# Performance work log

Measured on AMD Instinct MI355X. Metric: run time of the kernel, lower is better.

The kernel has to match this reference:

```python
import jax, jax.numpy as jnp
import numpy as np

B, N, D, H = 2, 2048, 1024, 16
HD = D // H

def rotate_half(x):
    # pairs (x1,x2) -> (-x2,x1), interleaved along last dim
    x1 = x[..., 0::2]
    x2 = x[..., 1::2]
    return jnp.stack((-x2, x1), axis=-1).reshape(x.shape)

def rope(freqs, t):
    return t * freqs[0] + rotate_half(t) * freqs[1]

def attn(q, k, v):
    scale = q.shape[-1] ** -0.5
    s = jnp.einsum('bhqd,bhkd->bhqk', q, k) * scale
    return jnp.einsum('bhqk,bhkd->bhqd', jax.nn.softmax(s, axis=-1), v)

def layernorm(x, g, b, eps=1e-5):
    m = x.mean(-1, keepdims=True)
    v = x.var(-1, keepdims=True)
    return (x - m) * jax.lax.rsqrt(v + eps) * g + b

def ffn(x, w1, b1, lg, lb, w2, b2):
    h = layernorm(x @ w1 + b1, lg, lb)
    return jax.nn.gelu(h, approximate=False) @ w2 + b2

def self_block(x, enc, wqkv_w, wqkv_b, out_w, out_b, f1w, f1b, lg, lb, f2w, f2b):
    b, n, d = x.shape
    hd = enc.shape[-1]; h = d // hd
    qkv = (x @ wqkv_w + wqkv_b).reshape(b, n, h, hd, 3).transpose(0, 2, 1, 3, 4)  # [b,h,n,hd,3]
    q, k, v = qkv[..., 0], qkv[..., 1], qkv[..., 2]
    q = rope(enc, q)
    k = rope(enc, k)
    ctx = attn(q, k, v).transpose(0, 2, 1, 3).reshape(b, n, d)
    msg = ctx @ out_w + out_b
    return x + ffn(jnp.concatenate([x, msg], -1), f1w, f1b, lg, lb, f2w, f2b)

def cross_block(x0, x1, h, qkw, qkb, vw, vb, ow, ob, f1w, f1b, lg, lb, f2w, f2b):
    b, n, d = x0.shape
    hd = d // h
    def heads(t):
        return t.reshape(b, -1, h, hd).transpose(0, 2, 1, 3)
    qk0 = heads(x0 @ qkw + qkb)
    qk1 = heads(x1 @ qkw + qkb)
    v0 = heads(x0 @ vw + vb)
    v1 = heads(x1 @ vw + vb)
    m0 = attn(qk0, qk1, v1).transpose(0, 2, 1, 3).reshape(b, n, d) @ ow + ob
    m1 = attn(qk1, qk0, v0).transpose(0, 2, 1, 3).reshape(b, n, d) @ ow + ob
    y0 = x0 + ffn(jnp.concatenate([x0, m0], -1), f1w, f1b, lg, lb, f2w, f2b)
    y1 = x1 + ffn(jnp.concatenate([x1, m1], -1), f1w, f1b, lg, lb, f2w, f2b)
    return y0, y1

def setup_inputs() -> dict:
    key = jax.random.key(0)
    ks = iter(jax.random.split(key, 40))
    def w(shape, scale=0.02):
        return (jax.random.normal(next(ks), shape, dtype=jnp.float32) * scale)
    inp = {
        'desc0': jax.random.normal(next(ks), (B, N, D), dtype=jnp.float32),
        'desc1': jax.random.normal(next(ks), (B, N, D), dtype=jnp.float32),
        'encoding0': jax.random.normal(next(ks), (2, B, 1, N, HD), dtype=jnp.float32),
        'encoding1': jax.random.normal(next(ks), (2, B, 1, N, HD), dtype=jnp.float32),
        # self-attention block params
        'wqkv_w': w((D, 3 * D)), 'wqkv_b': w((3 * D,)),
        'sout_w': w((D, D)), 'sout_b': w((D,)),
        'sf1_w': w((2 * D, 2 * D)), 'sf1_b': w((2 * D,)),
        'sln_g': jnp.ones((2 * D,), jnp.float32), 'sln_b': jnp.zeros((2 * D,), jnp.float32),
        'sf2_w': w((2 * D, D)), 'sf2_b': w((D,)),
        # cross-attention block params
        'qk_w': w((D, D)), 'qk_b': w((D,)),
        'v_w': w((D, D)), 'v_b': w((D,)),
        'cout_w': w((D, D)), 'cout_b': w((D,)),
        'cf1_w': w((2 * D, 2 * D)), 'cf1_b': w((2 * D,)),
        'cln_g': jnp.ones((2 * D,), jnp.float32), 'cln_b': jnp.zeros((2 * D,), jnp.float32),
        'cf2_w': w((2 * D, D)), 'cf2_b': w((D,)),
    }
    return inp

def reference(desc0, desc1, encoding0, encoding1,
              wqkv_w, wqkv_b, sout_w, sout_b, sf1_w, sf1_b, sln_g, sln_b, sf2_w, sf2_b,
              qk_w, qk_b, v_w, v_b, cout_w, cout_b, cf1_w, cf1_b, cln_g, cln_b, cf2_w, cf2_b):
    d0 = self_block(desc0, encoding0, wqkv_w, wqkv_b, sout_w, sout_b, sf1_w, sf1_b, sln_g, sln_b, sf2_w, sf2_b)
    d1 = self_block(desc1, encoding1, wqkv_w, wqkv_b, sout_w, sout_b, sf1_w, sf1_b, sln_g, sln_b, sf2_w, sf2_b)
    return cross_block(d0, d1, H, qk_w, qk_b, v_w, v_b, cout_w, cout_b, cf1_w, cf1_b, cln_g, cln_b, cf2_w, cf2_b)
```

## Files before the change

### kernel.cpp

```cpp
#include <hip/hip_runtime.h>


typedef unsigned short u16;
typedef unsigned int u32;
typedef float f32x4 __attribute__((ext_vector_type(4)));
typedef float f32x16 __attribute__((ext_vector_type(16)));
typedef __bf16 bf16x8 __attribute__((ext_vector_type(8)));
typedef u16 u16x2 __attribute__((ext_vector_type(2)));
typedef u16 u16x4 __attribute__((ext_vector_type(4)));
typedef u16 u16x8 __attribute__((ext_vector_type(8)));
typedef u32 u32x4 __attribute__((ext_vector_type(4)));

__device__ __forceinline__ u16 f2b(float f) {
  union { float f; unsigned u; } v; v.f = f;
  unsigned r = v.u + 0x7FFFu + ((v.u >> 16) & 1u);
  return (u16)(r >> 16);
}
__device__ __forceinline__ float b2f(u16 s) {
  union { unsigned u; float f; } v; v.u = ((unsigned)s) << 16;
  return v.f;
}
__device__ __forceinline__ void gload16(const void* g, void* l) {
  __builtin_amdgcn_global_load_lds((const __attribute__((address_space(1))) void*)g,
                                   (__attribute__((address_space(3))) void*)l, 16, 0, 0);
}
__device__ __forceinline__ u32 cvtpk(float lo, float hi) {
  u32 r;
  asm("v_cvt_pk_bf16_f32 %0, %1, %2" : "=v"(r) : "v"(lo), "v"(hi));
  return r;
}
#define MFMA16(a, b, c) __builtin_amdgcn_mfma_f32_16x16x32_bf16(a, b, c, 0, 0, 0)
#define MFMA32(a, b, c) __builtin_amdgcn_mfma_f32_32x32x16_bf16(a, b, c, 0, 0, 0)

__global__ __launch_bounds__(256) void wtrans(const float* __restrict__ src,
                                              u16* __restrict__ dst, int K, int N) {
  __shared__ __align__(16) u16 tile[64][72];
  const int k0 = blockIdx.y * 64, n0 = blockIdx.x * 64;
  const int t = threadIdx.x;
  {
    const int kl = t >> 2, nc = (t & 3) * 16;
    const float* sp = src + (size_t)(k0 + kl) * N + n0 + nc;
#pragma unroll
    for (int j = 0; j < 4; ++j) {
      float4 f = *(const float4*)(sp + j * 4);
      tile[kl][nc + j * 4 + 0] = f2b(f.x);
      tile[kl][nc + j * 4 + 1] = f2b(f.y);
      tile[kl][nc + j * 4 + 2] = f2b(f.z);
      tile[kl][nc + j * 4 + 3] = f2b(f.w);
    }
  }
  __syncthreads();
  {
    const int nl = t >> 2, kc = (t & 3) * 16;
    u16x8 o0, o1;
#pragma unroll
    for (int j = 0; j < 8; ++j) { o0[j] = tile[kc + j][nl]; o1[j] = tile[kc + 8 + j][nl]; }
    u16* dp = dst + (size_t)(n0 + nl) * K + k0 + kc;
    *(u16x8*)dp = o0;
    *(u16x8*)(dp + 8) = o1;
  }
}

__global__ void bias_cat2(const float* __restrict__ a, const float* __restrict__ b,
                          float* __restrict__ o) {
  int i = blockIdx.x * 256 + threadIdx.x;
  if (i < 2048) o[i] = (i < 1024) ? a[i] : b[i - 1024];
}

__global__ void prep_x(const float* __restrict__ d0, const float* __restrict__ d1,
                       u16* __restrict__ CAT) {
  size_t i4 = ((size_t)blockIdx.x * 256 + threadIdx.x) * 4;
  const float* src = (i4 < 4194304) ? (d0 + i4) : (d1 + (i4 - 4194304));
  float4 v = *(const float4*)src;
  size_t row = i4 >> 10, col = i4 & 1023;
  u16x4 o = {f2b(v.x), f2b(v.y), f2b(v.z), f2b(v.w)};
  *(u16x4*)(CAT + row * 2048 + col) = o;
}

template <int WF32, int WBF16, int RES>
__global__ __launch_bounds__(256) void gemm_bt(
    const u16* __restrict__ A, int lda, const u16* __restrict__ Bt, int ldb,
    const float* __restrict__ bias, int K, float* __restrict__ outf, int ldf,
    u16* __restrict__ outb, int ldob, int coloff, const float* __restrict__ res,
    const float* __restrict__ res2, int rsplit, int ldr) {
  __shared__ __align__(16) u16 As[128 * 32];
  __shared__ __align__(16) u16 Bs[128 * 32];
  const int m0 = blockIdx.y * 128, n0 = blockIdx.x * 128;
  const int t = threadIdx.x;
  const int w = t >> 6, l = t & 63;
  const int wr = (w >> 1) * 64, wc = (w & 1) * 64;
  const int lr = l & 15, lg = l >> 4;
  f32x4 acc[4][4] = {};
  const u16* Ab = A + (size_t)m0 * lda;
  const u16* Bb = Bt + (size_t)n0 * ldb;
  const int srow = t >> 2;
  const int scol = (t & 3) * 8;
  for (int k0 = 0; k0 < K; k0 += 32) {
    gload16(Ab + (size_t)srow * lda + k0 + scol, &As[srow * 32 + scol]);
    gload16(Ab + (size_t)(srow + 64) * lda + k0 + scol, &As[(srow + 64) * 32 + scol]);
    gload16(Bb + (size_t)srow * ldb + k0 + scol, &Bs[srow * 32 + scol]);
    gload16(Bb + (size_t)(srow + 64) * ldb + k0 + scol, &Bs[(srow + 64) * 32 + scol]);
    __syncthreads();
    bf16x8 af[4], bfr[4];
#pragma unroll
    for (int m = 0; m < 4; ++m) af[m] = *(const bf16x8*)&As[(wr + m * 16 + lr) * 32 + lg * 8];
#pragma unroll
    for (int n = 0; n < 4; ++n) bfr[n] = *(const bf16x8*)&Bs[(wc + n * 16 + lr) * 32 + lg * 8];
#pragma unroll
    for (int m = 0; m < 4; ++m)
#pragma unroll
      for (int n = 0; n < 4; ++n) acc[m][n] = MFMA16(af[m], bfr[n], acc[m][n]);
    __syncthreads();
  }
#pragma unroll
  for (int m = 0; m < 4; ++m) {
#pragma unroll
    for (int n = 0; n < 4; ++n) {
#pragma unroll
      for (int r = 0; r < 4; ++r) {
        const int row = m0 + wr + m * 16 + lg * 4 + r;
        const int col = n0 + wc + n * 16 + lr;
        float v = acc[m][n][r] + bias[col];
        if (RES) {
          const float* rp = res;
          int rr = row;
          if (row >= rsplit) { rp = res2; rr = row - rsplit; }
          v += rp[(size_t)rr * ldr + col];
        }
        if (WF32) outf[(size_t)row * ldf + col] = v;
        if (WBF16) outb[(size_t)row * ldob + coloff + col] = f2b(v);
      }
    }
  }
}

__global__ __launch_bounds__(256) void rope_split(
    const u16* __restrict__ QKV, const float* __restrict__ enc0,
    const float* __restrict__ enc1, u16* __restrict__ qo, u16* __restrict__ ko,
    u16* __restrict__ vo) {
  const int p = blockIdx.x, nt = blockIdx.y;
  const int bdb = p >> 4, h = p & 15;
  const int t = threadIdx.x;
  const int ip = t & 31, nl = t >> 5;
  const float* enc = (bdb < 2) ? enc0 : enc1;
  const float* e0base = enc + (size_t)(bdb & 1) * 131072 + ip * 2;
#pragma unroll 4
  for (int it = 0; it < 16; ++it) {
    const int n = nt * 128 + it * 8 + nl;
    const size_t row = (size_t)bdb * 2048 + n;
    const unsigned* su = (const unsigned*)(QKV + row * 3072 + h * 192 + ip * 6);
    const unsigned u0 = su[0], u1 = su[1], u2 = su[2];
    const float qe = b2f((u16)u0), ke = b2f((u16)(u0 >> 16));
    const u16 vbe = (u16)u1;
    const float qot = b2f((u16)(u1 >> 16));
    const float kot = b2f((u16)u2);
    const u16 vbo = (u16)(u2 >> 16);
    const float* ep = e0base + (size_t)n * 64;
    const float2 f0 = *(const float2*)ep;
    const float2 f1 = *(const float2*)(ep + 262144);
    u16x2 qw = {f2b(qe * f0.x - qot * f1.x), f2b(qot * f0.y + qe * f1.y)};
    u16x2 kw = {f2b(ke * f0.x - kot * f1.x), f2b(kot * f0.y + ke * f1.y)};
    u16x2 vw = {vbe, vbo};
    const size_t ob = row * 1024 + h * 64 + ip * 2;
    *(u16x2*)(qo + ob) = qw;
    *(u16x2*)(ko + ob) = kw;
    *(u16x2*)(vo + ob) = vw;
  }
}

__global__ __launch_bounds__(256) void vtrans(const u16* __restrict__ in, int in_ld,
                                              int col_off, u16* __restrict__ out) {
  const int p = blockIdx.x, nt = blockIdx.y;
  const int bdb = p >> 4, h = p & 15;
  const int t = threadIdx.x;
  __shared__ __align__(16) u16 tile[64][72];
  {
    const int nl = t >> 2, dc = (t & 3) * 16;
    const u16* sp = in + (size_t)(bdb * 2048 + nt * 64 + nl) * in_ld + col_off + h * 64 + dc;
    u16x8 a = *(const u16x8*)sp;
    u16x8 b = *(const u16x8*)(sp + 8);
#pragma unroll
    for (int j = 0; j < 8; ++j) { tile[nl][dc + j] = a[j]; tile[nl][dc + 8 + j] = b[j]; }
  }
  __syncthreads();
  {
    const int d = t >> 2, nc = (t & 3) * 16;
    u16x8 o0, o1;
#pragma unroll
    for (int j = 0; j < 8; ++j) { o0[j] = tile[nc + j][d]; o1[j] = tile[nc + 8 + j][d]; }
    u16* dp = out + (size_t)p * 131072 + (size_t)d * 2048 + nt * 64 + nc;
    *(u16x8*)dp = o0;
    *(u16x8*)(dp + 8) = o1;
  }
}

__global__ __launch_bounds__(256) void attn_fa(const u16* __restrict__ qbase, int q_ld,
                                               const u16* __restrict__ kbase, int k_ld,
                                               const u16* __restrict__ vtbase,
                                               u16* __restrict__ ctxbase, int mode) {
  const int qb = blockIdx.x;
  const int p = blockIdx.y;
  const int t = threadIdx.x, w = t >> 6, l = t & 63;
  const int lq = l & 31;
  const int hi = l >> 5;
  const int hi8 = hi * 8;

  const u16 *qp, *kp, *vtp;
  u16* op;
  if (mode == 0) {
    const int bdb = p >> 4, h = p & 15;
    const size_t rb = (size_t)bdb * 2048;
    qp = qbase + rb * q_ld + h * 64;
    kp = kbase + rb * k_ld + h * 64;
    vtp = vtbase + (size_t)p * 131072;
    op = ctxbase + rb * 1024 + h * 64;
  } else {
    const int bd = p >> 5, b = (p >> 4) & 1, h = p & 15;
    const size_t qrb = (size_t)bd * 4096 + (size_t)b * 2048;
    const size_t krb = (size_t)(1 - bd) * 4096 + (size_t)b * 2048;
    qp = qbase + qrb * q_ld + h * 64;
    kp = kbase + krb * k_ld + h * 64;
    const int pv = ((1 - bd) * 2 + b) * 16 + h;
    vtp = vtbase + (size_t)pv * 131072;
    op = ctxbase + qrb * 1024 + h * 64;
  }

  __shared__ __align__(16) u16 kbuf[2][64 * 64];
  __shared__ __align__(16) u16 vbuf[2][64 * 64];

  const int qrow = qb * 128 + w * 32 + lq;
  bf16x8 qf[4];
#pragma unroll
  for (int dc = 0; dc < 4; ++dc)
    qf[dc] = *(const bf16x8*)(qp + (size_t)qrow * q_ld + dc * 16 + hi8);

  f32x16 accO0 = {}, accO1 = {};
  float m2 = -1e30f, lrun = 0.f;
  const float SC = 0.18033688011116044f;

  const int sr0 = t >> 3;
  const int sc8 = ((t & 7) ^ (sr0 & 7)) * 8;
  const int ldst = sr0 * 64 + (t & 7) * 8;
  const int swz = (lq & 7) << 3;

  gload16(kp + (size_t)sr0 * k_ld + sc8, &kbuf[0][ldst]);
  gload16(kp + (size_t)(sr0 + 32) * k_ld + sc8, &kbuf[0][ldst + 2048]);
  gload16(vtp + (size_t)sr0 * 2048 + sc8, &vbuf[0][ldst]);
  gload16(vtp + (size_t)(sr0 + 32) * 2048 + sc8, &vbuf[0][ldst + 2048]);
  __syncthreads();

  for (int it = 0; it < 32; ++it) {
    const int cur = it & 1;
    if (it < 31) {
      const int kt = (it + 1) * 64;
      u16* kd = &kbuf[cur ^ 1][ldst];
      u16* vd = &vbuf[cur ^ 1][ldst];
      gload16(kp + (size_t)(kt + sr0) * k_ld + sc8, kd);
      gload16(kp + (size_t)(kt + sr0 + 32) * k_ld + sc8, kd + 2048);
      gload16(vtp + (size_t)sr0 * 2048 + kt + sc8, vd);
      gload16(vtp + (size_t)(sr0 + 32) * 2048 + kt + sc8, vd + 2048);
    }
    const u16* kb = kbuf[cur];
    const u16* vb = vbuf[cur];

    f32x16 s0 = {}, s1 = {};
    __builtin_amdgcn_s_setprio(1);
#pragma unroll
    for (int dc = 0; dc < 4; ++dc) {
      const int off = (dc * 16 + hi8) ^ swz;
      const bf16x8 ka0 = *(const bf16x8*)&kb[lq * 64 + off];
      const bf16x8 ka1 = *(const bf16x8*)&kb[(lq + 32) * 64 + off];
      s0 = MFMA32(ka0, qf[dc], s0);
      s1 = MFMA32(ka1, qf[dc], s1);
    }
    __builtin_amdgcn_s_setprio(0);

    float tm[8];
#pragma unroll
    for (int j = 0; j < 8; ++j)
      tm[j] = fmaxf(fmaxf(s0[j], s0[j + 8]), fmaxf(s1[j], s1[j + 8]));
    float mr = fmaxf(fmaxf(fmaxf(tm[0], tm[1]), fmaxf(tm[2], tm[3])),
                     fmaxf(fmaxf(tm[4], tm[5]), fmaxf(tm[6], tm[7])));
    mr = fmaxf(mr, __shfl_xor(mr, 32));
    const float m2new = fmaxf(m2, mr * SC);
    const float al = __builtin_amdgcn_exp2f(m2 - m2new);
    m2 = m2new;
    f32x16 p0, p1;
#pragma unroll
    for (int r = 0; r < 16; ++r) p0[r] = __builtin_amdgcn_exp2f(fmaf(s0[r], SC, -m2new));
#pragma unroll
    for (int r = 0; r < 16; ++r) p1[r] = __builtin_amdgcn_exp2f(fmaf(s1[r], SC, -m2new));
    const f32x16 ts = p0 + p1;
    float sa[8];
#pragma unroll
    for (int j = 0; j < 8; ++j) sa[j] = ts[j] + ts[j + 8];
    float rs = ((sa[0] + sa[1]) + (sa[2] + sa[3])) + ((sa[4] + sa[5]) + (sa[6] + sa[7]));
    rs += __shfl_xor(rs, 32);
    lrun = lrun * al + rs;
    accO0 *= al;
    accO1 *= al;

    bf16x8 paf[4];
#pragma unroll
    for (int kc = 0; kc < 4; ++kc) {
      const f32x16& ps = (kc < 2) ? p0 : p1;
      const int b0 = (kc & 1) * 8;
      u32 a = cvtpk(ps[b0 + 0], ps[b0 + 1]);
      u32 c = cvtpk(ps[b0 + 2], ps[b0 + 3]);
      u32 b = cvtpk(ps[b0 + 4], ps[b0 + 5]);
      u32 d = cvtpk(ps[b0 + 6], ps[b0 + 7]);
      asm("v_permlane32_swap_b32 %0, %1" : "+v"(a), "+v"(b));
      asm("v_permlane32_swap_b32 %0, %1" : "+v"(c), "+v"(d));
      u32x4 wv = {a, c, b, d};
      paf[kc] = __builtin_bit_cast(bf16x8, wv);
    }

    __builtin_amdgcn_s_setprio(1);
#pragma unroll
    for (int kc = 0; kc < 4; ++kc) {
      const int off = (kc * 16 + hi8) ^ swz;
      const bf16x8 va0 = *(const bf16x8*)&vb[lq * 64 + off];
      const bf16x8 va1 = *(const bf16x8*)&vb[(lq + 32) * 64 + off];
      accO0 = MFMA32(va0, paf[kc], accO0);
      accO1 = MFMA32(va1, paf[kc], accO1);
    }
    __builtin_amdgcn_s_setprio(0);
    __syncthreads();
  }

  const float inv = 1.f / lrun;
  accO0 *= inv;
  accO1 *= inv;
  u16* orow = op + (size_t)qrow * 1024;
#pragma unroll
  for (int r = 0; r < 16; r += 2) {
    const int d = (r & 3) + 8 * (r >> 2) + 4 * hi;
    *(u32*)&orow[d] = cvtpk(accO0[r], accO0[r + 1]);
    *(u32*)&orow[d + 32] = cvtpk(accO1[r], accO1[r + 1]);
  }
}

__global__ __launch_bounds__(256) void ln_gelu(const u16* __restrict__ H,
                                               const float* __restrict__ gam,
                                               const float* __restrict__ bet,
                                               u16* __restrict__ G) {
  const int row = blockIdx.x, t = threadIdx.x;
  u16x8 hv = *(const u16x8*)(H + (size_t)row * 2048 + t * 8);
  float v[8];
#pragma unroll
  for (int j = 0; j < 8; ++j) v[j] = b2f(hv[j]);
  float s = 0.f, s2 = 0.f;
#pragma unroll
  for (int j = 0; j < 8; ++j) { s += v[j]; s2 += v[j] * v[j]; }
#pragma unroll
  for (int off = 32; off; off >>= 1) { s += __shfl_xor(s, off); s2 += __shfl_xor(s2, off); }
  __shared__ float red[8];
  const int w = t >> 6, l = t & 63;
  if (l == 0) { red[w] = s; red[4 + w] = s2; }
  __syncthreads();
  s = red[0] + red[1] + red[2] + red[3];
  s2 = red[4] + red[5] + red[6] + red[7];
  const float mean = s * (1.f / 2048.f);
  const float rstd = rsqrtf(s2 * (1.f / 2048.f) - mean * mean + 1e-5f);
  u16x8 o;
#pragma unroll
  for (int j = 0; j < 8; ++j) {
    const int col = t * 8 + j;
    const float x = (v[j] - mean) * rstd * gam[col] + bet[col];
    o[j] = f2b(x * 0.5f * (1.f + erff(x * 0.7071067811865475f)));
  }
  *(u16x8*)(G + (size_t)row * 2048 + t * 8) = o;
}

extern "C" void kernel_launch(void* const* d_in, const int* in_sizes, int n_in,
                              void* d_out, int out_size, void* d_ws, size_t ws_size,
                              hipStream_t stream) {
  (void)in_sizes; (void)n_in; (void)out_size; (void)ws_size;
  const float* desc0 = (const float*)d_in[0];
  const float* desc1 = (const float*)d_in[1];
  const float* enc0 = (const float*)d_in[2];
  const float* enc1 = (const float*)d_in[3];
  const float* wqkv_w = (const float*)d_in[4];
  const float* wqkv_b = (const float*)d_in[5];
  const float* sout_w = (const float*)d_in[6];
  const float* sout_b = (const float*)d_in[7];
  const float* sf1_w = (const float*)d_in[8];
  const float* sf1_b = (const float*)d_in[9];
  const float* sln_g = (const float*)d_in[10];
  const float* sln_b = (const float*)d_in[11];
  const float* sf2_w = (const float*)d_in[12];
  const float* sf2_b = (const float*)d_in[13];
  const float* qk_w = (const float*)d_in[14];
  const float* qk_b = (const float*)d_in[15];
  const float* v_w = (const float*)d_in[16];
  const float* v_b = (const float*)d_in[17];
  const float* cout_w = (const float*)d_in[18];
  const float* cout_b = (const float*)d_in[19];
  const float* cf1_w = (const float*)d_in[20];
  const float* cf1_b = (const float*)d_in[21];
  const float* cln_g = (const float*)d_in[22];
  const float* cln_b = (const float*)d_in[23];
  const float* cf2_w = (const float*)d_in[24];
  const float* cf2_b = (const float*)d_in[25];

  char* ws = (char*)d_ws;
  size_t off = 0;
  auto alloc = [&](size_t n) { char* r = ws + off; off += (n + 255) & ~(size_t)255; return r; };
  u16* wqkv_t = (u16*)alloc((size_t)3072 * 1024 * 2);
  u16* sout_t = (u16*)alloc((size_t)1024 * 1024 * 2);
  u16* sf1_t = (u16*)alloc((size_t)2048 * 2048 * 2);
  u16* sf2_t = (u16*)alloc((size_t)1024 * 2048 * 2);
  u16* wcat_t = (u16*)alloc((size_t)2048 * 1024 * 2);
  u16* cout_t = (u16*)alloc((size_t)1024 * 1024 * 2);
  u16* cf1_t = (u16*)alloc((size_t)2048 * 2048 * 2);
  u16* cf2_t = (u16*)alloc((size_t)1024 * 2048 * 2);
  float* biascat = (float*)alloc(2048 * 4);
  u16* CATb = (u16*)alloc((size_t)8192 * 2048 * 2);
  char* BIG = alloc((size_t)8192 * 3072 * 2);
  char* QKB = alloc((size_t)3 * 8192 * 1024 * 2);
  u16* VT = (u16*)alloc((size_t)64 * 64 * 2048 * 2);

  u16* QKVbf = (u16*)BIG;
  u16* Hbf = (u16*)BIG;
  u16* CQKV = (u16*)BIG;
  u16* qB = (u16*)QKB;
  u16* kB = qB + (size_t)8192 * 1024;
  u16* vB = kB + (size_t)8192 * 1024;
  u16* G = (u16*)QKB;
  u16* CTX = vB;
  float* OUT = (float*)d_out;

  hipStream_t st = stream;
  wtrans<<<dim3(48, 16), 256, 0, st>>>(wqkv_w, wqkv_t, 1024, 3072);
  wtrans<<<dim3(16, 16), 256, 0, st>>>(sout_w, sout_t, 1024, 1024);
  wtrans<<<dim3(32, 32), 256, 0, st>>>(sf1_w, sf1_t, 2048, 2048);
  wtrans<<<dim3(16, 32), 256, 0, st>>>(sf2_w, sf2_t, 2048, 1024);
  wtrans<<<dim3(16, 16), 256, 0, st>>>(qk_w, wcat_t, 1024, 1024);
  wtrans<<<dim3(16, 16), 256, 0, st>>>(v_w, wcat_t + (size_t)1024 * 1024, 1024, 1024);
  wtrans<<<dim3(16, 16), 256, 0, st>>>(cout_w, cout_t, 1024, 1024);
  wtrans<<<dim3(32, 32), 256, 0, st>>>(cf1_w, cf1_t, 2048, 2048);
  wtrans<<<dim3(16, 32), 256, 0, st>>>(cf2_w, cf2_t, 2048, 1024);
  bias_cat2<<<8, 256, 0, st>>>(qk_b, v_b, biascat);
  prep_x<<<8192, 256, 0, st>>>(desc0, desc1, CATb);

  gemm_bt<0, 1, 0><<<dim3(24, 64), 256, 0, st>>>(CATb, 2048, wqkv_t, 1024, wqkv_b, 1024,
                                                 nullptr, 0, QKVbf, 3072, 0, nullptr,
                                                 nullptr, 1 << 30, 0);
  rope_split<<<dim3(64, 16), 256, 0, st>>>(QKVbf, enc0, enc1, qB, kB, vB);
  vtrans<<<dim3(64, 32), 256, 0, st>>>(vB, 1024, 0, VT);
  attn_fa<<<dim3(16, 64), 256, 0, st>>>(qB, 1024, kB, 1024, VT, CTX, 0);
  gemm_bt<0, 1, 0><<<dim3(8, 64), 256, 0, st>>>(CTX, 1024, sout_t, 1024, sout_b, 1024,
                                                nullptr, 0, CATb, 2048, 1024, nullptr,
                                                nullptr, 1 << 30, 0);
  gemm_bt<0, 1, 0><<<dim3(16, 64), 256, 0, st>>>(CATb, 2048, sf1_t, 2048, sf1_b, 2048,
                                                 nullptr, 0, Hbf, 2048, 0, nullptr,
                                                 nullptr, 1 << 30, 0);
  ln_gelu<<<8192, 256, 0, st>>>(Hbf, sln_g, sln_b, G);
  gemm_bt<1, 1, 1><<<dim3(8, 64), 256, 0, st>>>(G, 2048, sf2_t, 2048, sf2_b, 2048,
                                                OUT, 1024, CATb, 2048, 0, desc0,
                                                desc1, 4096, 1024);

  gemm_bt<0, 1, 0><<<dim3(16, 64), 256, 0, st>>>(CATb, 2048, wcat_t, 1024, biascat, 1024,
                                                 nullptr, 0, CQKV, 2048, 0, nullptr,
                                                 nullptr, 1 << 30, 0);
  vtrans<<<dim3(64, 32), 256, 0, st>>>(CQKV, 2048, 1024, VT);
  attn_fa<<<dim3(16, 64), 256, 0, st>>>(CQKV, 2048, CQKV, 2048, VT, CTX, 1);
  gemm_bt<0, 1, 0><<<dim3(8, 64), 256, 0, st>>>(CTX, 1024, cout_t, 1024, cout_b, 1024,
                                                nullptr, 0, CATb, 2048, 1024, nullptr,
                                                nullptr, 1 << 30, 0);
  gemm_bt<0, 1, 0><<<dim3(16, 64), 256, 0, st>>>(CATb, 2048, cf1_t, 2048, cf1_b, 2048,
                                                 nullptr, 0, Hbf, 2048, 0, nullptr,
                                                 nullptr, 1 << 30, 0);
  ln_gelu<<<8192, 256, 0, st>>>(Hbf, cln_g, cln_b, G);
  gemm_bt<1, 0, 1><<<dim3(8, 64), 256, 0, st>>>(G, 2048, cf2_t, 2048, cf2_b, 2048,
                                                OUT, 1024, nullptr, 0, 0, OUT,
                                                OUT, 1 << 30, 1024);
}
```

Measured before the change: 1.147 ms.

## Replace GEMM with 256-row tiled, triple-buffered, swizzled 512-thread kernel

Replaces the single-buffered 128x128 bf16 GEMM with an 8-wave kernel that uses 256xBN tiles (BN 256 or 128) and a three-stage LDS ring. Global-to-LDS loads are issued two k-steps ahead and gated with explicit vmcnt waits, so one barrier per step replaces two. An XOR swizzle on LDS columns targets bank conflicts, and a block-ID remap groups workgroups for L2 locality. The larger tiles and bigger register footprint lower occupancy and leave fewer workgroups per GEMM, which may under-fill the chip on the smaller shapes.

New measurement: 1.026 ms. -10.6%, faster.

```diff
diff --git a/kernel.cpp b/kernel.cpp
--- a/kernel.cpp
+++ b/kernel.cpp
@@ -29,6 +29,11 @@
   asm("v_cvt_pk_bf16_f32 %0, %1, %2" : "=v"(r) : "v"(lo), "v"(hi));
   return r;
 }
+template <int N> __device__ __forceinline__ void waitvm() {
+  if constexpr (N == 0) asm volatile("s_waitcnt vmcnt(0)" ::: "memory");
+  else if constexpr (N == 3) asm volatile("s_waitcnt vmcnt(3)" ::: "memory");
+  else asm volatile("s_waitcnt vmcnt(4)" ::: "memory");
+}
 #define MFMA16(a, b, c) __builtin_amdgcn_mfma_f32_16x16x32_bf16(a, b, c, 0, 0, 0)
 #define MFMA32(a, b, c) __builtin_amdgcn_mfma_f32_32x32x16_bf16(a, b, c, 0, 0, 0)
 
@@ -77,49 +82,88 @@
   *(u16x4*)(CAT + row * 2048 + col) = o;
 }
 
-template <int WF32, int WBF16, int RES>
-__global__ __launch_bounds__(256) void gemm_bt(
+template <int BN, int WF32, int WBF16, int RES>
+__global__ __launch_bounds__(512, 2) void gemm8(
     const u16* __restrict__ A, int lda, const u16* __restrict__ Bt, int ldb,
-    const float* __restrict__ bias, int K, float* __restrict__ outf, int ldf,
-    u16* __restrict__ outb, int ldob, int coloff, const float* __restrict__ res,
-    const float* __restrict__ res2, int rsplit, int ldr) {
-  __shared__ __align__(16) u16 As[128 * 32];
-  __shared__ __align__(16) u16 Bs[128 * 32];
-  const int m0 = blockIdx.y * 128, n0 = blockIdx.x * 128;
+    const float* __restrict__ bias, int K, float* outf, int ldf,
+    u16* __restrict__ outb, int ldob, int coloff, const float* res,
+    const float* res2, int rsplit, int ldr) {
+  constexpr int ASZ = 256 * 32;
+  constexpr int BSZ = BN * 32;
+  constexpr int BUF = ASZ + BSZ;
+  constexpr int L = (BN == 256) ? 4 : 3;
+  constexpr int NR = BN / 64;
+  __shared__ __align__(16) u16 lds[3 * BUF];
+
+  const int gx = gridDim.x, nwg = gx * gridDim.y;
+  int id = blockIdx.y * gx + blockIdx.x;
+  id = (id & 7) * (nwg >> 3) + (id >> 3);
+  const int bx = id % gx, by = id / gx;
+  const int m0 = by * 256, n0 = bx * BN;
+
   const int t = threadIdx.x;
   const int w = t >> 6, l = t & 63;
-  const int wr = (w >> 1) * 64, wc = (w & 1) * 64;
+  const int wm = w >> 2, wn = w & 3;
   const int lr = l & 15, lg = l >> 4;
-  f32x4 acc[4][4] = {};
-  const u16* Ab = A + (size_t)m0 * lda;
-  const u16* Bb = Bt + (size_t)n0 * ldb;
-  const int srow = t >> 2;
-  const int scol = (t & 3) * 8;
-  for (int k0 = 0; k0 < K; k0 += 32) {
-    gload16(Ab + (size_t)srow * lda + k0 + scol, &As[srow * 32 + scol]);
-    gload16(Ab + (size_t)(srow + 64) * lda + k0 + scol, &As[(srow + 64) * 32 + scol]);
-    gload16(Bb + (size_t)srow * ldb + k0 + scol, &Bs[srow * 32 + scol]);
-    gload16(Bb + (size_t)(srow + 64) * ldb + k0 + scol, &Bs[(srow + 64) * 32 + scol]);
-    __syncthreads();
-    bf16x8 af[4], bfr[4];
-#pragma unroll
-    for (int m = 0; m < 4; ++m) af[m] = *(const bf16x8*)&As[(wr + m * 16 + lr) * 32 + lg * 8];
-#pragma unroll
-    for (int n = 0; n < 4; ++n) bfr[n] = *(const bf16x8*)&Bs[(wc + n * 16 + lr) * 32 + lg * 8];
-#pragma unroll
-    for (int m = 0; m < 4; ++m)
-#pragma unroll
-      for (int n = 0; n < 4; ++n) acc[m][n] = MFMA16(af[m], bfr[n], acc[m][n]);
-    __syncthreads();
-  }
-#pragma unroll
-  for (int m = 0; m < 4; ++m) {
-#pragma unroll
-    for (int n = 0; n < 4; ++n) {
+
+  const int r4 = t >> 2, s4 = t & 3;
+  const int ssw = ((s4 ^ ((r4 >> 1) & 3)) * 8);
+  const int dst = r4 * 32 + s4 * 8;
+  const u16* Abase = A + (size_t)m0 * lda;
+  const u16* Bbase = Bt + (size_t)n0 * ldb;
+
+  auto stage = [&](int tt, u16* buf) {
+    const int k0 = tt * 32;
+    gload16(Abase + (size_t)r4 * lda + k0 + ssw, buf + dst);
+    gload16(Abase + (size_t)(r4 + 128) * lda + k0 + ssw, buf + dst + 128 * 32);
+    u16* bb = buf + ASZ;
+    gload16(Bbase + (size_t)r4 * ldb + k0 + ssw, bb + dst);
+    if constexpr (BN == 256)
+      gload16(Bbase + (size_t)(r4 + 128) * ldb + k0 + ssw, bb + dst + 128 * 32);
+  };
+
+  const int cA = (lg ^ ((lr >> 1) & 3)) * 8;
+  f32x4 acc[8][NR] = {};
+  const int nt = K >> 5;
+
+  stage(0, lds);
+  stage(1, lds + BUF);
+  waitvm<L>();
+  __builtin_amdgcn_s_barrier();
+
+  for (int tt = 0; tt < nt; ++tt) {
+    u16* buf = lds + (tt % 3) * BUF;
+    if (tt + 2 < nt) stage(tt + 2, lds + ((tt + 2) % 3) * BUF);
+    const u16* As = buf;
+    const u16* Bs = buf + ASZ;
+    bf16x8 af[8], bfr[NR];
+#pragma unroll
+    for (int m = 0; m < 8; ++m)
+      af[m] = *(const bf16x8*)&As[(wm * 128 + m * 16 + lr) * 32 + cA];
+#pragma unroll
+    for (int n = 0; n < NR; ++n)
+      bfr[n] = *(const bf16x8*)&Bs[(wn * (NR * 16) + n * 16 + lr) * 32 + cA];
+#pragma unroll
+    for (int m = 0; m < 8; ++m)
+#pragma unroll
+      for (int n = 0; n < NR; ++n) acc[m][n] = MFMA16(af[m], bfr[n], acc[m][n]);
+    if (tt + 2 < nt) {
+      waitvm<L>();
+      __builtin_amdgcn_s_barrier();
+    } else if (tt + 1 < nt) {
+      waitvm<0>();
+      __builtin_amdgcn_s_barrier();
+    }
+  }
+
+#pragma unroll
+  for (int m = 0; m < 8; ++m) {
+#pragma unroll
+    for (int n = 0; n < NR; ++n) {
 #pragma unroll
       for (int r = 0; r < 4; ++r) {
-        const int row = m0 + wr + m * 16 + lg * 4 + r;
-        const int col = n0 + wc + n * 16 + lr;
+        const int row = m0 + wm * 128 + m * 16 + lg * 4 + r;
+        const int col = n0 + wn * (NR * 16) + n * 16 + lr;
         float v = acc[m][n][r] + bias[col];
         if (RES) {
           const float* rp = res;
@@ -443,36 +487,36 @@
   bias_cat2<<<8, 256, 0, st>>>(qk_b, v_b, biascat);
   prep_x<<<8192, 256, 0, st>>>(desc0, desc1, CATb);
 
-  gemm_bt<0, 1, 0><<<dim3(24, 64), 256, 0, st>>>(CATb, 2048, wqkv_t, 1024, wqkv_b, 1024,
-                                                 nullptr, 0, QKVbf, 3072, 0, nullptr,
-                                                 nullptr, 1 << 30, 0);
+  gemm8<256, 0, 1, 0><<<dim3(12, 32), 512, 0, st>>>(CATb, 2048, wqkv_t, 1024, wqkv_b,
+                                                    1024, nullptr, 0, QKVbf, 3072, 0,
+                                                    nullptr, nullptr, 1 << 30, 0);
   rope_split<<<dim3(64, 16), 256, 0, st>>>(QKVbf, enc0, enc1, qB, kB, vB);
   vtrans<<<dim3(64, 32), 256, 0, st>>>(vB, 1024, 0, VT);
   attn_fa<<<dim3(16, 64), 256, 0, st>>>(qB, 1024, kB, 1024, VT, CTX, 0);
-  gemm_bt<0, 1, 0><<<dim3(8, 64), 256, 0, st>>>(CTX, 1024, sout_t, 1024, sout_b, 1024,
-                                                nullptr, 0, CATb, 2048, 1024, nullptr,
-                                                nullptr, 1 << 30, 0);
-  gemm_bt<0, 1, 0><<<dim3(16, 64), 256, 0, st>>>(CATb, 2048, sf1_t, 2048, sf1_b, 2048,
-                                                 nullptr, 0, Hbf, 2048, 0, nullptr,
-                                                 nullptr, 1 << 30, 0);
+  gemm8<128, 0, 1, 0><<<dim3(8, 32), 512, 0, st>>>(CTX, 1024, sout_t, 1024, sout_b,
+                                                   1024, nullptr, 0, CATb, 2048, 1024,
+                                                   nullptr, nullptr, 1 << 30, 0);
+  gemm8<256, 0, 1, 0><<<dim3(8, 32), 512, 0, st>>>(CATb, 2048, sf1_t, 2048, sf1_b,
+                                                   2048, nullptr, 0, Hbf, 2048, 0,
+                                                   nullptr, nullptr, 1 << 30, 0);
   ln_gelu<<<8192, 256, 0, st>>>(Hbf, sln_g, sln_b, G);
-  gemm_bt<1, 1, 1><<<dim3(8, 64), 256, 0, st>>>(G, 2048, sf2_t, 2048, sf2_b, 2048,
-                                                OUT, 1024, CATb, 2048, 0, desc0,
-                                                desc1, 4096, 1024);
-
-  gemm_bt<0, 1, 0><<<dim3(16, 64), 256, 0, st>>>(CATb, 2048, wcat_t, 1024, biascat, 1024,
-                                                 nullptr, 0, CQKV, 2048, 0, nullptr,
-                                                 nullptr, 1 << 30, 0);
+  gemm8<128, 1, 1, 1><<<dim3(8, 32), 512, 0, st>>>(G, 2048, sf2_t, 2048, sf2_b, 2048,
+                                                   OUT, 1024, CATb, 2048, 0, desc0,
+                                                   desc1, 4096, 1024);
+
+  gemm8<256, 0, 1, 0><<<dim3(8, 32), 512, 0, st>>>(CATb, 2048, wcat_t, 1024, biascat,
+                                                   1024, nullptr, 0, CQKV, 2048, 0,
+                                                   nullptr, nullptr, 1 << 30, 0);
   vtrans<<<dim3(64, 32), 256, 0, st>>>(CQKV, 2048, 1024, VT);
   attn_fa<<<dim3(16, 64), 256, 0, st>>>(CQKV, 2048, CQKV, 2048, VT, CTX, 1);
-  gemm_bt<0, 1, 0><<<dim3(8, 64), 256, 0, st>>>(CTX, 1024, cout_t, 1024, cout_b, 1024,
-                                                nullptr, 0, CATb, 2048, 1024, nullptr,
-                                                nullptr, 1 << 30, 0);
-  gemm_bt<0, 1, 0><<<dim3(16, 64), 256, 0, st>>>(CATb, 2048, cf1_t, 2048, cf1_b, 2048,
-                                                 nullptr, 0, Hbf, 2048, 0, nullptr,
-                                                 nullptr, 1 << 30, 0);
+  gemm8<128, 0, 1, 0><<<dim3(8, 32), 512, 0, st>>>(CTX, 1024, cout_t, 1024, cout_b,
+                                                   1024, nullptr, 0, CATb, 2048, 1024,
+                                                   nullptr, nullptr, 1 << 30, 0);
+  gemm8<256, 0, 1, 0><<<dim3(8, 32), 512, 0, st>>>(CATb, 2048, cf1_t, 2048, cf1_b,
+                                                   2048, nullptr, 0, Hbf, 2048, 0,
+                                                   nullptr, nullptr, 1 << 30, 0);
   ln_gelu<<<8192, 256, 0, st>>>(Hbf, cln_g, cln_b, G);
-  gemm_bt<1, 0, 1><<<dim3(8, 64), 256, 0, st>>>(G, 2048, cf2_t, 2048, cf2_b, 2048,
-                                                OUT, 1024, nullptr, 0, 0, OUT,
-                                                OUT, 1 << 30, 1024);
-}
+  gemm8<128, 1, 0, 1><<<dim3(8, 32), 512, 0, st>>>(G, 2048, cf2_t, 2048, cf2_b, 2048,
+                                                   OUT, 1024, nullptr, 0, 0, OUT, OUT,
+                                                   1 << 30, 1024);
+}
```
